# Kernel tuning notes

Hardware: AMD Instinct MI355X
Metric: run time of the kernel (lower is better)

Reference implementation:

```python
import jax, jax.numpy as jnp
import numpy as np

N_NODES = 100000
N_EDGES = 600000
IN_FEATS = 128
OUT_FEATS = 128
BN_EPS = 1e-5


def setup_inputs() -> dict:
    key = jax.random.key(0)
    ks = jax.random.split(key, 8)
    x = jax.random.normal(ks[0], (N_NODES, IN_FEATS), dtype=jnp.float32)
    edge_index = jax.random.randint(ks[1], (2, N_EDGES), 0, N_NODES, dtype=jnp.int64)
    # GCNConv linear weight (no bias in lin), bias added after aggregation
    W = jax.random.normal(ks[2], (IN_FEATS, OUT_FEATS), dtype=jnp.float32) / np.sqrt(IN_FEATS)
    b = jax.random.normal(ks[3], (OUT_FEATS,), dtype=jnp.float32) * 0.01
    # BatchNorm affine params
    gamma = jnp.ones((OUT_FEATS,), dtype=jnp.float32)
    beta = jnp.zeros((OUT_FEATS,), dtype=jnp.float32)
    # residual Linear: y = x @ W_res + b_res (W_res stored [in, out])
    W_res = jax.random.normal(ks[4], (IN_FEATS, OUT_FEATS), dtype=jnp.float32) / np.sqrt(IN_FEATS)
    b_res = jax.random.normal(ks[5], (OUT_FEATS,), dtype=jnp.float32) * 0.01
    return {"x": x, "edge_index": edge_index, "W": W, "b": b,
            "gamma": gamma, "beta": beta, "W_res": W_res, "b_res": b_res}


def _gcn_forward(x, edge_index, W, b, gamma, beta, W_res, b_res):
    n = x.shape[0]
    # --- GCNConv (PyG defaults): add self-loops, symmetric normalization ---
    loops = jnp.arange(n, dtype=edge_index.dtype)
    row = jnp.concatenate([edge_index[0], loops])  # source nodes
    col = jnp.concatenate([edge_index[1], loops])  # destination nodes
    deg = jax.ops.segment_sum(jnp.ones_like(col, dtype=x.dtype), col, num_segments=n)
    dinv = jax.lax.rsqrt(deg)  # deg >= 1 thanks to self-loops
    norm = dinv[row] * dinv[col]  # [E+N]
    h = x @ W  # [N, out]
    msg = h[row] * norm[:, None]  # gather + scale, [E+N, out]
    agg = jax.ops.segment_sum(msg, col, num_segments=n) + b  # scatter-add + bias
    # --- ReLU + BatchNorm (training mode, biased variance) ---
    r = jax.nn.relu(agg)
    mean = jnp.mean(r, axis=0)
    var = jnp.mean(jnp.square(r - mean), axis=0)
    bn = gamma * (r - mean) * jax.lax.rsqrt(var + BN_EPS) + beta
    # --- residual dense path ---
    res = x @ W_res + b_res
    return bn + res


def reference(x, edge_index, W, b, gamma, beta, W_res, b_res):
    return _gcn_forward(x, edge_index, W, b, gamma, beta, W_res, b_res)
```

## Files before the change

kernel.cpp:

```cpp
#include <hip/hip_runtime.h>

#define NN 100000
#define NE 600000
#define F  128
#define BN_EPS 1e-5f
#define TM 128
#define TK 32

__global__ void k_init(const unsigned* __restrict__ ei, int* __restrict__ flag,
                       int* __restrict__ cnt, float* __restrict__ colsum, float* __restrict__ colsq)
{
    int i = blockIdx.x * 256 + threadIdx.x;
    if (i <= NN) cnt[i] = 0;
    if (i < F) { colsum[i] = 0.f; colsq[i] = 0.f; }
    if (blockIdx.x == 0) {
        __shared__ int any;
        if (threadIdx.x == 0) any = 0;
        __syncthreads();
        unsigned v = ei[2 * threadIdx.x + 1];
        if (v != 0u) atomicOr(&any, 1);
        __syncthreads();
        if (threadIdx.x == 0) *flag = (any == 0) ? 1 : 0;
    }
}

__global__ void k_count(const void* __restrict__ ei, const int* __restrict__ flag, int* __restrict__ cnt)
{
    int e = blockIdx.x * 256 + threadIdx.x;
    if (e >= NE) return;
    int col;
    if (*flag) col = (int)((const long long*)ei)[NE + e];
    else       col = ((const int*)ei)[NE + e];
    atomicAdd(&cnt[col], 1);
}

__global__ void k_bsum(const int* __restrict__ cnt, int* __restrict__ bsum)
{
    __shared__ int s[256];
    int b = blockIdx.x, t = threadIdx.x;
    int i = b * 256 + t;
    s[t] = (i <= NN) ? cnt[i] : 0;
    __syncthreads();
    for (int o = 128; o > 0; o >>= 1) {
        if (t < o) s[t] += s[t + o];
        __syncthreads();
    }
    if (t == 0) bsum[b] = s[0];
}

__global__ void k_bscan(const int* __restrict__ bsum, int* __restrict__ bbase)
{
    __shared__ int s[512];
    int t = threadIdx.x;
    int v = (t < 391) ? bsum[t] : 0;
    s[t] = v;
    __syncthreads();
    for (int o = 1; o < 512; o <<= 1) {
        int tmp = (t >= o) ? s[t - o] : 0;
        __syncthreads();
        s[t] += tmp;
        __syncthreads();
    }
    if (t < 391) bbase[t] = s[t] - v;
}

__global__ void k_offsets(const int* __restrict__ cnt, const int* __restrict__ bbase,
                          int* __restrict__ off, int* __restrict__ cur,
                          float* __restrict__ dinv)
{
    __shared__ int s[256];
    int b = blockIdx.x, t = threadIdx.x;
    int i = b * 256 + t;
    int v = (i <= NN) ? cnt[i] : 0;
    s[t] = v;
    __syncthreads();
    for (int o = 1; o < 256; o <<= 1) {
        int tmp = (t >= o) ? s[t - o] : 0;
        __syncthreads();
        s[t] += tmp;
        __syncthreads();
    }
    int excl = s[t] - v + bbase[b];
    if (i <= NN) {
        off[i] = excl;
        if (i < NN) {
            cur[i] = excl;
            float d = (float)(v + 1);
            float r = rsqrtf(d);
            r = r * (1.5f - 0.5f * d * r * r);
            dinv[i] = r;
        }
    }
}

__global__ void k_place(const void* __restrict__ ei, const int* __restrict__ flag,
                        int* __restrict__ cur, int* __restrict__ csr)
{
    int e = blockIdx.x * 256 + threadIdx.x;
    if (e >= NE) return;
    int row, col;
    if (*flag) {
        row = (int)((const long long*)ei)[e];
        col = (int)((const long long*)ei)[NE + e];
    } else {
        row = ((const int*)ei)[e];
        col = ((const int*)ei)[NE + e];
    }
    int slot = atomicAdd(&cur[col], 1);
    csr[slot] = row;
}

__global__ __launch_bounds__(256) void k_agg(const float* __restrict__ x, const float* __restrict__ dinv,
                                             const int* __restrict__ off, const int* __restrict__ csr,
                                             float* __restrict__ aggx)
{
    int node = blockIdx.x * 4 + (threadIdx.x >> 6);
    int lane = threadIdx.x & 63;
    int sub  = lane & 31;
    int half = lane >> 5;
    float ax = 0.f, ay = 0.f, az = 0.f, aw = 0.f;
    int e0 = off[node], e1 = off[node + 1];
    int e = e0 + half;
    for (; e + 2 < e1; e += 4) {
        int r0 = csr[e], r1 = csr[e + 2];
        float s0 = dinv[r0], s1 = dinv[r1];
        float4 u0 = ((const float4*)(x + (size_t)r0 * F))[sub];
        float4 u1 = ((const float4*)(x + (size_t)r1 * F))[sub];
        ax = fmaf(u0.x, s0, ax); ay = fmaf(u0.y, s0, ay);
        az = fmaf(u0.z, s0, az); aw = fmaf(u0.w, s0, aw);
        ax = fmaf(u1.x, s1, ax); ay = fmaf(u1.y, s1, ay);
        az = fmaf(u1.z, s1, az); aw = fmaf(u1.w, s1, aw);
    }
    for (; e < e1; e += 2) {
        int r = csr[e]; float s = dinv[r];
        float4 u = ((const float4*)(x + (size_t)r * F))[sub];
        ax = fmaf(u.x, s, ax); ay = fmaf(u.y, s, ay);
        az = fmaf(u.z, s, az); aw = fmaf(u.w, s, aw);
    }
    ax += __shfl_xor(ax, 32); ay += __shfl_xor(ay, 32);
    az += __shfl_xor(az, 32); aw += __shfl_xor(aw, 32);
    if (half == 0) {
        float di = dinv[node];
        float4 v = ((const float4*)(x + (size_t)node * F))[sub];
        float4 o;
        o.x = (fmaf(v.x, di, ax)) * di;
        o.y = (fmaf(v.y, di, ay)) * di;
        o.z = (fmaf(v.z, di, az)) * di;
        o.w = (fmaf(v.w, di, aw)) * di;
        ((float4*)(aggx + (size_t)node * F))[sub] = o;
    }
}

__global__ __launch_bounds__(256, 2) void k_gemm2(
    float* __restrict__ A, const float* __restrict__ X,
    const float* __restrict__ W, const float* __restrict__ Wr,
    const float* __restrict__ bias, const float* __restrict__ biasr,
    float* __restrict__ out, float* __restrict__ colsum, float* __restrict__ colsq)
{
    __shared__ float At[TM][TK];
    __shared__ float Wt[TK][F];

    const int tid = threadIdx.x;
    const int tx = tid & 31;
    const int ty = tid >> 5;
    const int type = blockIdx.y;
    const int r0 = blockIdx.x * TM;
    const float* __restrict__ src = type ? X : (const float*)A;
    const float* __restrict__ wm  = type ? Wr : W;

    const int arow = tid >> 3;
    const int aslot = (tid & 7) << 2;
    const int wrow = tid >> 5;
    const int wcol = (tid & 31) << 2;

    float4 ra[4], rw[4];
#pragma unroll
    for (int it = 0; it < 4; ++it) {
        int gr = r0 + arow + it * 32;
        ra[it] = make_float4(0.f, 0.f, 0.f, 0.f);
        if (gr < NN) ra[it] = *(const float4*)(src + (size_t)gr * F + aslot);
    }
#pragma unroll
    for (int it = 0; it < 4; ++it)
        rw[it] = *(const float4*)(wm + (size_t)(wrow + it * 8) * F + wcol);

    float4 acc[16];
#pragma unroll
    for (int i = 0; i < 16; ++i) acc[i] = make_float4(0.f, 0.f, 0.f, 0.f);

    for (int kc = 0; kc < 4; ++kc) {
        __syncthreads();
#pragma unroll
        for (int it = 0; it < 4; ++it)
            *(float4*)(&At[arow + it * 32][aslot]) = ra[it];
#pragma unroll
        for (int it = 0; it < 4; ++it)
            *(float4*)(&Wt[wrow + it * 8][wcol]) = rw[it];
        __syncthreads();
        if (kc < 3) {
            const int kb = (kc + 1) * TK;
#pragma unroll
            for (int it = 0; it < 4; ++it) {
                int gr = r0 + arow + it * 32;
                ra[it] = make_float4(0.f, 0.f, 0.f, 0.f);
                if (gr < NN) ra[it] = *(const float4*)(src + (size_t)gr * F + kb + aslot);
            }
#pragma unroll
            for (int it = 0; it < 4; ++it)
                rw[it] = *(const float4*)(wm + (size_t)(kb + wrow + it * 8) * F + wcol);
        }
#pragma unroll
        for (int kq = 0; kq < 8; ++kq) {
            float4 w0 = *(const float4*)(&Wt[kq * 4 + 0][tx * 4]);
            float4 w1 = *(const float4*)(&Wt[kq * 4 + 1][tx * 4]);
            float4 w2 = *(const float4*)(&Wt[kq * 4 + 2][tx * 4]);
            float4 w3 = *(const float4*)(&Wt[kq * 4 + 3][tx * 4]);
#pragma unroll
            for (int i = 0; i < 16; ++i) {
                float4 a = *(const float4*)(&At[ty * 16 + i][kq * 4]);
                acc[i].x = fmaf(a.x, w0.x, acc[i].x);
                acc[i].y = fmaf(a.x, w0.y, acc[i].y);
                acc[i].z = fmaf(a.x, w0.z, acc[i].z);
                acc[i].w = fmaf(a.x, w0.w, acc[i].w);
                acc[i].x = fmaf(a.y, w1.x, acc[i].x);
                acc[i].y = fmaf(a.y, w1.y, acc[i].y);
                acc[i].z = fmaf(a.y, w1.z, acc[i].z);
                acc[i].w = fmaf(a.y, w1.w, acc[i].w);
                acc[i].x = fmaf(a.z, w2.x, acc[i].x);
                acc[i].y = fmaf(a.z, w2.y, acc[i].y);
                acc[i].z = fmaf(a.z, w2.z, acc[i].z);
                acc[i].w = fmaf(a.z, w2.w, acc[i].w);
                acc[i].x = fmaf(a.w, w3.x, acc[i].x);
                acc[i].y = fmaf(a.w, w3.y, acc[i].y);
                acc[i].z = fmaf(a.w, w3.z, acc[i].z);
                acc[i].w = fmaf(a.w, w3.w, acc[i].w);
            }
        }
    }
    __syncthreads();

    if (type == 0) {
        float* ssum = &Wt[0][0];
        float* ssq  = &Wt[0][0] + F;
        if (tid < 256) ((float*)&Wt[0][0])[tid] = 0.f;
        __syncthreads();
        float4 bv = *(const float4*)(bias + tx * 4);
        float ls[4] = {0.f, 0.f, 0.f, 0.f};
        float lq[4] = {0.f, 0.f, 0.f, 0.f};
#pragma unroll
        for (int i = 0; i < 16; ++i) {
            int gr = r0 + ty * 16 + i;
            if (gr < NN) {
                float r0_ = fmaxf(acc[i].x + bv.x, 0.f);
                float r1_ = fmaxf(acc[i].y + bv.y, 0.f);
                float r2_ = fmaxf(acc[i].z + bv.z, 0.f);
                float r3_ = fmaxf(acc[i].w + bv.w, 0.f);
                ls[0] += r0_; lq[0] = fmaf(r0_, r0_, lq[0]);
                ls[1] += r1_; lq[1] = fmaf(r1_, r1_, lq[1]);
                ls[2] += r2_; lq[2] = fmaf(r2_, r2_, lq[2]);
                ls[3] += r3_; lq[3] = fmaf(r3_, r3_, lq[3]);
                *(float4*)(A + (size_t)gr * F + tx * 4) = make_float4(r0_, r1_, r2_, r3_);
            }
        }
#pragma unroll
        for (int j = 0; j < 4; ++j) {
            atomicAdd(&ssum[tx * 4 + j], ls[j]);
            atomicAdd(&ssq[tx * 4 + j], lq[j]);
        }
        __syncthreads();
        if (tid < F) {
            atomicAdd(&colsum[tid], ssum[tid]);
            atomicAdd(&colsq[tid], ssq[tid]);
        }
    } else {
        float4 bv = *(const float4*)(biasr + tx * 4);
#pragma unroll
        for (int i = 0; i < 16; ++i) {
            int gr = r0 + ty * 16 + i;
            if (gr < NN) {
                *(float4*)(out + (size_t)gr * F + tx * 4) =
                    make_float4(acc[i].x + bv.x, acc[i].y + bv.y,
                                acc[i].z + bv.z, acc[i].w + bv.w);
            }
        }
    }
}

__global__ void k_stats(const float* __restrict__ colsum, const float* __restrict__ colsq,
                        const float* __restrict__ gamma, const float* __restrict__ beta,
                        float* __restrict__ scale, float* __restrict__ shift)
{
    int c = threadIdx.x;
    if (c < F) {
        float inv_n = 1.0f / (float)NN;
        float mean = colsum[c] * inv_n;
        float ex2  = colsq[c] * inv_n;
        float var  = fmaxf(ex2 - mean * mean, 0.f);
        float d = var + BN_EPS;
        float is = rsqrtf(d);
        is = is * (1.5f - 0.5f * d * is * is);
        float sc = gamma[c] * is;
        scale[c] = sc;
        shift[c] = beta[c] - sc * mean;
    }
}

__global__ __launch_bounds__(256) void k_final(const float* __restrict__ r,
                                               const float* __restrict__ scale,
                                               const float* __restrict__ shift,
                                               float* __restrict__ out)
{
    int idx = blockIdx.x * 256 + threadIdx.x;
    int c4 = idx & 31;
    float4 rv = ((const float4*)r)[idx];
    float4 ov = ((float4*)out)[idx];
    float4 sv = ((const float4*)scale)[c4];
    float4 hv = ((const float4*)shift)[c4];
    float4 o;
    o.x = fmaf(rv.x, sv.x, hv.x) + ov.x;
    o.y = fmaf(rv.y, sv.y, hv.y) + ov.y;
    o.z = fmaf(rv.z, sv.z, hv.z) + ov.z;
    o.w = fmaf(rv.w, sv.w, hv.w) + ov.w;
    ((float4*)out)[idx] = o;
}

extern "C" void kernel_launch(void* const* d_in, const int* in_sizes, int n_in,
                              void* d_out, int out_size, void* d_ws, size_t ws_size,
                              hipStream_t stream)
{
    (void)in_sizes; (void)n_in; (void)out_size; (void)ws_size;
    const float* x     = (const float*)d_in[0];
    const void*  ei    = d_in[1];
    const float* W     = (const float*)d_in[2];
    const float* b     = (const float*)d_in[3];
    const float* gamma = (const float*)d_in[4];
    const float* beta  = (const float*)d_in[5];
    const float* Wres  = (const float*)d_in[6];
    const float* bres  = (const float*)d_in[7];
    float* out = (float*)d_out;

    char* w = (char*)d_ws;
    float* aggx   = (float*)(w + 0);
    int*   cnt    = (int*)  (w + 51200000);
    float* dinv   = (float*)(w + 51600128);
    int*   off    = (int*)  (w + 52000256);
    int*   cur    = (int*)  (w + 52400384);
    int*   csr    = (int*)  (w + 52800512);
    int*   bsum   = (int*)  (w + 55200512);
    int*   bbase  = (int*)  (w + 55202176);
    float* colsum = (float*)(w + 55203840);
    float* colsq  = (float*)(w + 55204352);
    float* scale  = (float*)(w + 55204864);
    float* shift  = (float*)(w + 55205376);
    int*   flag   = (int*)  (w + 55205888);

    const int G_INIT = 392;
    const int G_E    = (NE + 255) / 256;
    const int G_N    = 391;
    const int G_AGG  = NN / 4;
    const dim3 G_GEMM((NN + TM - 1) / TM, 2);
    const int G_FIN  = (NN * F / 4) / 256;

    k_init   <<<G_INIT, 256, 0, stream>>>((const unsigned*)ei, flag, cnt, colsum, colsq);
    k_count  <<<G_E, 256, 0, stream>>>(ei, flag, cnt);
    k_bsum   <<<G_N, 256, 0, stream>>>(cnt, bsum);
    k_bscan  <<<1, 512, 0, stream>>>(bsum, bbase);
    k_offsets<<<G_N, 256, 0, stream>>>(cnt, bbase, off, cur, dinv);
    k_place  <<<G_E, 256, 0, stream>>>(ei, flag, cur, csr);
    k_agg    <<<G_AGG, 256, 0, stream>>>(x, dinv, off, csr, aggx);
    k_gemm2  <<<G_GEMM, 256, 0, stream>>>(aggx, x, W, Wres, b, bres, out, colsum, colsq);
    k_stats  <<<1, 128, 0, stream>>>(colsum, colsq, gamma, beta, scale, shift);
    k_final  <<<G_FIN, 256, 0, stream>>>(aggx, scale, shift, out);
}
```

Baseline: 372.2 us.

## Use split-bf16 MFMA for dense GEMMs with prepacked weight fragments

```diff
diff --git a/kernel.cpp b/kernel.cpp
--- a/kernel.cpp
+++ b/kernel.cpp
@@ -6,6 +6,20 @@
 #define BN_EPS 1e-5f
 #define TM 128
 #define TK 32
+
+typedef short bf8 __attribute__((ext_vector_type(8)));
+typedef float f32x4 __attribute__((ext_vector_type(4)));
+
+__device__ __forceinline__ unsigned short bf16_rne(float x) {
+    unsigned u = __float_as_uint(x);
+    return (unsigned short)((u + 0x7FFFu + ((u >> 16) & 1u)) >> 16);
+}
+__device__ __forceinline__ void split_bf16(float x, unsigned short& h, unsigned short& l) {
+    unsigned short hh = bf16_rne(x);
+    float hf = __uint_as_float(((unsigned)hh) << 16);
+    h = hh;
+    l = bf16_rne(x - hf);
+}
 
 __global__ void k_init(const unsigned* __restrict__ ei, int* __restrict__ flag,
                        int* __restrict__ cnt, float* __restrict__ colsum, float* __restrict__ colsq)
@@ -108,6 +122,26 @@
     }
     int slot = atomicAdd(&cur[col], 1);
     csr[slot] = row;
+}
+
+__global__ void k_wprep(const float* __restrict__ W, const float* __restrict__ Wr,
+                        unsigned short* __restrict__ wprep)
+{
+    int t = blockIdx.x * 256 + threadIdx.x;
+    int lane = t & 63;
+    int nf   = (t >> 6) & 7;
+    int c    = (t >> 9) & 3;
+    int type = t >> 11;
+    const float* wsrc = type ? Wr : W;
+    int col = nf * 16 + (lane & 15);
+    int k0  = c * 32 + (lane >> 4) * 8;
+    unsigned short hi[8], lo[8];
+#pragma unroll
+    for (int j = 0; j < 8; ++j)
+        split_bf16(wsrc[(size_t)(k0 + j) * F + col], hi[j], lo[j]);
+    unsigned short* dst = wprep + (size_t)t * 16;
+#pragma unroll
+    for (int j = 0; j < 8; ++j) { dst[j] = hi[j]; dst[8 + j] = lo[j]; }
 }
 
 __global__ __launch_bounds__(256) void k_agg(const float* __restrict__ x, const float* __restrict__ dinv,
@@ -151,138 +185,139 @@
     }
 }
 
-__global__ __launch_bounds__(256, 2) void k_gemm2(
+__global__ __launch_bounds__(256) void k_gemm2(
     float* __restrict__ A, const float* __restrict__ X,
-    const float* __restrict__ W, const float* __restrict__ Wr,
+    const unsigned short* __restrict__ wprep,
     const float* __restrict__ bias, const float* __restrict__ biasr,
     float* __restrict__ out, float* __restrict__ colsum, float* __restrict__ colsq)
 {
-    __shared__ float At[TM][TK];
-    __shared__ float Wt[TK][F];
-
-    const int tid = threadIdx.x;
-    const int tx = tid & 31;
-    const int ty = tid >> 5;
+    __shared__ unsigned short Ahi[TM][40];
+    __shared__ unsigned short Alo[TM][40];
+    __shared__ float sstat[256];
+
+    const int tid  = threadIdx.x;
     const int type = blockIdx.y;
-    const int r0 = blockIdx.x * TM;
+    const int r0   = blockIdx.x * TM;
     const float* __restrict__ src = type ? X : (const float*)A;
-    const float* __restrict__ wm  = type ? Wr : W;
-
-    const int arow = tid >> 3;
+
+    const int lane = tid & 63;
+    const int wv = tid >> 6;
+    const int wr = wv >> 1;
+    const int wc = wv & 1;
+    const int l15 = lane & 15;
+    const int lq4 = lane >> 4;
+    const int k0  = lq4 * 8;
+
+    const int arow  = tid >> 3;
     const int aslot = (tid & 7) << 2;
-    const int wrow = tid >> 5;
-    const int wcol = (tid & 31) << 2;
-
-    float4 ra[4], rw[4];
+
+    float4 ra[4];
 #pragma unroll
     for (int it = 0; it < 4; ++it) {
         int gr = r0 + arow + it * 32;
         ra[it] = make_float4(0.f, 0.f, 0.f, 0.f);
         if (gr < NN) ra[it] = *(const float4*)(src + (size_t)gr * F + aslot);
     }
-#pragma unroll
-    for (int it = 0; it < 4; ++it)
-        rw[it] = *(const float4*)(wm + (size_t)(wrow + it * 8) * F + wcol);
-
-    float4 acc[16];
-#pragma unroll
-    for (int i = 0; i < 16; ++i) acc[i] = make_float4(0.f, 0.f, 0.f, 0.f);
-
-    for (int kc = 0; kc < 4; ++kc) {
-        __syncthreads();
-#pragma unroll
-        for (int it = 0; it < 4; ++it)
-            *(float4*)(&At[arow + it * 32][aslot]) = ra[it];
-#pragma unroll
-        for (int it = 0; it < 4; ++it)
-            *(float4*)(&Wt[wrow + it * 8][wcol]) = rw[it];
-        __syncthreads();
-        if (kc < 3) {
-            const int kb = (kc + 1) * TK;
+
+    f32x4 acc[4][4];
+#pragma unroll
+    for (int m = 0; m < 4; ++m)
+#pragma unroll
+        for (int n = 0; n < 4; ++n) acc[m][n] = (f32x4){0.f, 0.f, 0.f, 0.f};
+
+    for (int c = 0; c < 4; ++c) {
+        __syncthreads();
+#pragma unroll
+        for (int it = 0; it < 4; ++it) {
+            int row = arow + it * 32;
+            unsigned short h0, h1, h2, h3, l0, l1, l2, l3;
+            split_bf16(ra[it].x, h0, l0); split_bf16(ra[it].y, h1, l1);
+            split_bf16(ra[it].z, h2, l2); split_bf16(ra[it].w, h3, l3);
+            *(ushort4*)&Ahi[row][aslot] = make_ushort4(h0, h1, h2, h3);
+            *(ushort4*)&Alo[row][aslot] = make_ushort4(l0, l1, l2, l3);
+        }
+        __syncthreads();
+        if (c < 3) {
+            int kb = (c + 1) * TK;
 #pragma unroll
             for (int it = 0; it < 4; ++it) {
                 int gr = r0 + arow + it * 32;
                 ra[it] = make_float4(0.f, 0.f, 0.f, 0.f);
                 if (gr < NN) ra[it] = *(const float4*)(src + (size_t)gr * F + kb + aslot);
             }
-#pragma unroll
-            for (int it = 0; it < 4; ++it)
-                rw[it] = *(const float4*)(wm + (size_t)(kb + wrow + it * 8) * F + wcol);
-        }
-#pragma unroll
-        for (int kq = 0; kq < 8; ++kq) {
-            float4 w0 = *(const float4*)(&Wt[kq * 4 + 0][tx * 4]);
-            float4 w1 = *(const float4*)(&Wt[kq * 4 + 1][tx * 4]);
-            float4 w2 = *(const float4*)(&Wt[kq * 4 + 2][tx * 4]);
-            float4 w3 = *(const float4*)(&Wt[kq * 4 + 3][tx * 4]);
-#pragma unroll
-            for (int i = 0; i < 16; ++i) {
-                float4 a = *(const float4*)(&At[ty * 16 + i][kq * 4]);
-                acc[i].x = fmaf(a.x, w0.x, acc[i].x);
-                acc[i].y = fmaf(a.x, w0.y, acc[i].y);
-                acc[i].z = fmaf(a.x, w0.z, acc[i].z);
-                acc[i].w = fmaf(a.x, w0.w, acc[i].w);
-                acc[i].x = fmaf(a.y, w1.x, acc[i].x);
-                acc[i].y = fmaf(a.y, w1.y, acc[i].y);
-                acc[i].z = fmaf(a.y, w1.z, acc[i].z);
-                acc[i].w = fmaf(a.y, w1.w, acc[i].w);
-                acc[i].x = fmaf(a.z, w2.x, acc[i].x);
-                acc[i].y = fmaf(a.z, w2.y, acc[i].y);
-                acc[i].z = fmaf(a.z, w2.z, acc[i].z);
-                acc[i].w = fmaf(a.z, w2.w, acc[i].w);
-                acc[i].x = fmaf(a.w, w3.x, acc[i].x);
-                acc[i].y = fmaf(a.w, w3.y, acc[i].y);
-                acc[i].z = fmaf(a.w, w3.z, acc[i].z);
-                acc[i].w = fmaf(a.w, w3.w, acc[i].w);
+        }
+        bf8 bhi[4], blo[4];
+#pragma unroll
+        for (int n = 0; n < 4; ++n) {
+            int entry = ((type * 4 + c) * 8 + wc * 4 + n) * 64 + lane;
+            const bf8* pb = (const bf8*)(wprep + (size_t)entry * 16);
+            bhi[n] = pb[0];
+            blo[n] = pb[1];
+        }
+#pragma unroll
+        for (int m = 0; m < 4; ++m) {
+            int row = wr * 64 + m * 16 + l15;
+            bf8 ah = *(const bf8*)&Ahi[row][k0];
+            bf8 al = *(const bf8*)&Alo[row][k0];
+#pragma unroll
+            for (int n = 0; n < 4; ++n) {
+                acc[m][n] = __builtin_amdgcn_mfma_f32_16x16x32_bf16(ah, bhi[n], acc[m][n], 0, 0, 0);
+                acc[m][n] = __builtin_amdgcn_mfma_f32_16x16x32_bf16(ah, blo[n], acc[m][n], 0, 0, 0);
+                acc[m][n] = __builtin_amdgcn_mfma_f32_16x16x32_bf16(al, bhi[n], acc[m][n], 0, 0, 0);
             }
         }
     }
     __syncthreads();
 
     if (type == 0) {
-        float* ssum = &Wt[0][0];
-        float* ssq  = &Wt[0][0] + F;
-        if (tid < 256) ((float*)&Wt[0][0])[tid] = 0.f;
-        __syncthreads();
-        float4 bv = *(const float4*)(bias + tx * 4);
+        sstat[tid] = 0.f;
+        __syncthreads();
+        float bv[4];
+#pragma unroll
+        for (int n = 0; n < 4; ++n) bv[n] = bias[wc * 64 + n * 16 + l15];
         float ls[4] = {0.f, 0.f, 0.f, 0.f};
         float lq[4] = {0.f, 0.f, 0.f, 0.f};
 #pragma unroll
-        for (int i = 0; i < 16; ++i) {
-            int gr = r0 + ty * 16 + i;
-            if (gr < NN) {
-                float r0_ = fmaxf(acc[i].x + bv.x, 0.f);
-                float r1_ = fmaxf(acc[i].y + bv.y, 0.f);
-                float r2_ = fmaxf(acc[i].z + bv.z, 0.f);
-                float r3_ = fmaxf(acc[i].w + bv.w, 0.f);
-                ls[0] += r0_; lq[0] = fmaf(r0_, r0_, lq[0]);
-                ls[1] += r1_; lq[1] = fmaf(r1_, r1_, lq[1]);
-                ls[2] += r2_; lq[2] = fmaf(r2_, r2_, lq[2]);
-                ls[3] += r3_; lq[3] = fmaf(r3_, r3_, lq[3]);
-                *(float4*)(A + (size_t)gr * F + tx * 4) = make_float4(r0_, r1_, r2_, r3_);
+        for (int m = 0; m < 4; ++m)
+#pragma unroll
+            for (int reg = 0; reg < 4; ++reg) {
+                int gr = r0 + wr * 64 + m * 16 + lq4 * 4 + reg;
+                if (gr < NN) {
+#pragma unroll
+                    for (int n = 0; n < 4; ++n) {
+                        float r = fmaxf(acc[m][n][reg] + bv[n], 0.f);
+                        A[(size_t)gr * F + wc * 64 + n * 16 + l15] = r;
+                        ls[n] += r;
+                        lq[n] = fmaf(r, r, lq[n]);
+                    }
+                }
             }
-        }
-#pragma unroll
-        for (int j = 0; j < 4; ++j) {
-            atomicAdd(&ssum[tx * 4 + j], ls[j]);
-            atomicAdd(&ssq[tx * 4 + j], lq[j]);
+#pragma unroll
+        for (int n = 0; n < 4; ++n) {
+            int col = wc * 64 + n * 16 + l15;
+            atomicAdd(&sstat[col], ls[n]);
+            atomicAdd(&sstat[128 + col], lq[n]);
         }
         __syncthreads();
         if (tid < F) {
-            atomicAdd(&colsum[tid], ssum[tid]);
-            atomicAdd(&colsq[tid], ssq[tid]);
+            atomicAdd(&colsum[tid], sstat[tid]);
+            atomicAdd(&colsq[tid], sstat[128 + tid]);
         }
     } else {
-        float4 bv = *(const float4*)(biasr + tx * 4);
-#pragma unroll
-        for (int i = 0; i < 16; ++i) {
-            int gr = r0 + ty * 16 + i;
-            if (gr < NN) {
-                *(float4*)(out + (size_t)gr * F + tx * 4) =
-                    make_float4(acc[i].x + bv.x, acc[i].y + bv.y,
-                                acc[i].z + bv.z, acc[i].w + bv.w);
+        float bv[4];
+#pragma unroll
+        for (int n = 0; n < 4; ++n) bv[n] = biasr[wc * 64 + n * 16 + l15];
+#pragma unroll
+        for (int m = 0; m < 4; ++m)
+#pragma unroll
+            for (int reg = 0; reg < 4; ++reg) {
+                int gr = r0 + wr * 64 + m * 16 + lq4 * 4 + reg;
+                if (gr < NN) {
+#pragma unroll
+                    for (int n = 0; n < 4; ++n)
+                        out[(size_t)gr * F + wc * 64 + n * 16 + l15] = acc[m][n][reg] + bv[n];
+                }
             }
-        }
     }
 }
 
@@ -342,6 +377,7 @@
     char* w = (char*)d_ws;
     float* aggx   = (float*)(w + 0);
     int*   cnt    = (int*)  (w + 51200000);
+    unsigned short* wprep = (unsigned short*)(w + 51200000);
     float* dinv   = (float*)(w + 51600128);
     int*   off    = (int*)  (w + 52000256);
     int*   cur    = (int*)  (w + 52400384);
@@ -367,8 +403,9 @@
     k_bscan  <<<1, 512, 0, stream>>>(bsum, bbase);
     k_offsets<<<G_N, 256, 0, stream>>>(cnt, bbase, off, cur, dinv);
     k_place  <<<G_E, 256, 0, stream>>>(ei, flag, cur, csr);
+    k_wprep  <<<16, 256, 0, stream>>>(W, Wres, wprep);
     k_agg    <<<G_AGG, 256, 0, stream>>>(x, dinv, off, csr, aggx);
-    k_gemm2  <<<G_GEMM, 256, 0, stream>>>(aggx, x, W, Wres, b, bres, out, colsum, colsq);
+    k_gemm2  <<<G_GEMM, 256, 0, stream>>>(aggx, x, wprep, b, bres, out, colsum, colsq);
     k_stats  <<<1, 128, 0, stream>>>(colsum, colsq, gamma, beta, scale, shift);
     k_final  <<<G_FIN, 256, 0, stream>>>(aggx, scale, shift, out);
 }
```

New measurement: 318.6 us. 14.4% less time.
